# Kernel tuning notes

Measured on AMD Instinct MI355X. Metric: run time of the kernel, lower is better.

The kernel has to match this reference:

```python
import jax, jax.numpy as jnp
import numpy as np

I_T = 0.5       # IoU threshold self.I_t
GAMMA = 2.0     # focal loss gamma
EPS = 1e-7      # focal loss eps clamp
BS, P, C_IN = 8, 2048, 512


def pairwise_iou(b):
    # b: (bs, P, 4) xyxy -> (bs, P, P), same math as torchvision box_iou (no +1)
    area = (b[..., 2] - b[..., 0]) * (b[..., 3] - b[..., 1])
    lt = jnp.maximum(b[:, :, None, :2], b[:, None, :, :2])
    rb = jnp.minimum(b[:, :, None, 2:], b[:, None, :, 2:])
    wh = jnp.clip(rb - lt, 0.0, None)
    inter = wh[..., 0] * wh[..., 1]
    return inter / (area[:, :, None] + area[:, None, :] - inter)


def assign_labels_weights(pre_score, labels, rois):
    # Vectorized, order-faithful version of the per-batch/per-class python loop.
    # Selected seeds per class c: proposals with pre_score[...,c] > 0.5 if more than
    # one, else the single argmax proposal (torch code falls back when k<=1).
    # Sequential `_I > old` running max over (c, j) in ascending order is equivalent
    # to a global first-occurrence argmax (strict >), so per-class max + running
    # compare with earlier-class tie preference reproduces it exactly.
    bs, Pn = pre_score.shape[0], pre_score.shape[1]
    iou = pairwise_iou(rois)                      # (bs, P, P)
    run_I = jnp.full((bs, Pn), -1.0, pre_score.dtype)
    run_w = jnp.ones((bs, Pn), pre_score.dtype)
    hits = []
    for c in range(3):
        s = pre_score[:, :, c]                    # (bs, P)
        th = s > 0.5
        cnt = th.sum(-1)
        onehot = jnp.arange(Pn)[None, :] == jnp.argmax(s, -1)[:, None]
        sel = jnp.where((cnt > 1)[:, None], th, onehot)
        sel = sel & (labels[:, c] != 0)[:, None]  # skip classes absent from image
        masked = jnp.where(sel[:, None, :], iou, -2.0)  # (bs, P, P)
        val = masked.max(-1)                      # best IoU vs any seed of class c
        jidx = masked.argmax(-1)
        cand_x = jnp.take_along_axis(s, jidx, axis=1)
        better = val > run_I
        run_w = jnp.where(better, cand_x, run_w)
        run_I = jnp.where(better, val, run_I)
        hits.append(val > I_T)
    hit = jnp.stack(hits, -1)                     # (bs, P, 3)
    bg = (~hit.any(-1))[..., None]
    y = jnp.concatenate([hit.astype(pre_score.dtype), bg.astype(pre_score.dtype)], -1)
    return y, run_w


def icr_forward(inputs, fc_w, fc_b, pre_score, labels, rois, num):
    bs = inputs.shape[0] // num
    xr = inputs @ fc_w + fc_b                     # (bs*P, 4)
    logit = jax.nn.softmax(xr.reshape(bs, num, 4), -1)
    ps = jax.lax.stop_gradient(pre_score)         # .clone().detach()
    lb = jax.lax.stop_gradient(labels)
    y, w = assign_labels_weights(ps, lb, rois)
    y = y.reshape(bs * num, 4)
    w = w.reshape(bs * num, 1)
    # FocalLoss(gamma=2, mode='none')
    p = jnp.clip(jax.nn.softmax(xr, -1), EPS, 1.0 - EPS)
    fl = -y * jnp.log(p) * (1.0 - p) ** GAMMA
    imbalance = y.sum(0)                          # (4,)
    loss = (w * fl / (imbalance + 1e-7)).reshape(bs, num, 4)
    lab = lb.at[:, 3].set(1.0)[:, None, :]        # lab[:,0,3]=1
    w_ = 10.0 * jnp.exp(logit) * (1.0 - lab) + lab
    loss = (loss * w_).sum() / bs
    return logit, loss


def setup_inputs():
    key = jax.random.key(0)
    k = jax.random.split(key, 6)
    inputs = jax.random.normal(k[0], (BS * P, C_IN), jnp.float32)
    fc_w = jax.random.normal(k[1], (C_IN, 4), jnp.float32) * 0.02
    fc_b = jnp.zeros((4,), jnp.float32)
    pre_score = jax.random.uniform(k[2], (BS, P, 4), dtype=jnp.float32)
    labels = (jax.random.uniform(k[3], (BS, 4)) < 0.5).astype(jnp.float32)
    labels = labels.at[:, 3].set(0.0)
    xy = jax.random.uniform(k[4], (BS, P, 2), dtype=jnp.float32) * 448.0
    wh = jax.random.uniform(k[5], (BS, P, 2), dtype=jnp.float32) * 63.0 + 1.0
    rois = jnp.concatenate([xy, xy + wh], -1)     # valid xyxy boxes in 512x512
    return {"inputs": inputs, "fc_w": fc_w, "fc_b": fc_b, "pre_score": pre_score,
            "labels": labels, "rois": rois, "num": P}


def reference(inputs, fc_w, fc_b, pre_score, labels, rois, num):
    return icr_forward(inputs, fc_w, fc_b, pre_score, labels, rois, num)
```

## Files before the change

kernel.cpp:

```cpp
#include <hip/hip_runtime.h>

#define BSZ 8
#define PN  2048
#define CIN 512
#define CAP 2048


__global__ __launch_bounds__(256) void k_front(
    const float* __restrict__ inp, const float* __restrict__ fcw,
    const float* __restrict__ fcb, const float* __restrict__ ps,
    const float* __restrict__ labels, const float* __restrict__ rois,
    float* __restrict__ logit, float* __restrict__ accum,
    int* __restrict__ meta, float* __restrict__ sList,
    float4* __restrict__ roiList)
{
  const int t = threadIdx.x;
  if (blockIdx.x >= 24) {
    const int gw   = (((int)blockIdx.x - 24) * 256 + t) >> 6;
    const int lane = t & 63;
    const int kb   = lane << 2;
    const float4 wa0 = *(const float4*)(fcw + (kb + 0) * 4);
    const float4 wa1 = *(const float4*)(fcw + (kb + 1) * 4);
    const float4 wa2 = *(const float4*)(fcw + (kb + 2) * 4);
    const float4 wa3 = *(const float4*)(fcw + (kb + 3) * 4);
    const float4 wb0 = *(const float4*)(fcw + (256 + kb + 0) * 4);
    const float4 wb1 = *(const float4*)(fcw + (256 + kb + 1) * 4);
    const float4 wb2 = *(const float4*)(fcw + (256 + kb + 2) * 4);
    const float4 wb3 = *(const float4*)(fcw + (256 + kb + 3) * 4);
    const float4 bias = *(const float4*)fcb;
    #pragma unroll
    for (int rr = 0; rr < 4; ++rr) {
      const int r = (gw << 2) + rr;
      const float* row = inp + r * CIN;
      const float4 xa = *(const float4*)(row + kb);
      const float4 xb = *(const float4*)(row + 256 + kb);
      float a0 = xa.x*wa0.x + xa.y*wa1.x + xa.z*wa2.x + xa.w*wa3.x
               + xb.x*wb0.x + xb.y*wb1.x + xb.z*wb2.x + xb.w*wb3.x;
      float a1 = xa.x*wa0.y + xa.y*wa1.y + xa.z*wa2.y + xa.w*wa3.y
               + xb.x*wb0.y + xb.y*wb1.y + xb.z*wb2.y + xb.w*wb3.y;
      float a2 = xa.x*wa0.z + xa.y*wa1.z + xa.z*wa2.z + xa.w*wa3.z
               + xb.x*wb0.z + xb.y*wb1.z + xb.z*wb2.z + xb.w*wb3.z;
      float a3 = xa.x*wa0.w + xa.y*wa1.w + xa.z*wa2.w + xa.w*wa3.w
               + xb.x*wb0.w + xb.y*wb1.w + xb.z*wb2.w + xb.w*wb3.w;
      #pragma unroll
      for (int off = 32; off; off >>= 1) {
        a0 += __shfl_xor(a0, off); a1 += __shfl_xor(a1, off);
        a2 += __shfl_xor(a2, off); a3 += __shfl_xor(a3, off);
      }
      if (lane == 0) {
        a0 += bias.x; a1 += bias.y; a2 += bias.z; a3 += bias.w;
        const float m  = fmaxf(fmaxf(a0, a1), fmaxf(a2, a3));
        const float e0 = expf(a0 - m), e1 = expf(a1 - m);
        const float e2 = expf(a2 - m), e3 = expf(a3 - m);
        const float inv = 1.0f / (e0 + e1 + e2 + e3);
        float4 o; o.x = e0*inv; o.y = e1*inv; o.z = e2*inv; o.w = e3*inv;
        *(float4*)(logit + r * 4) = o;
      }
    }
    return;
  }

  const int bc = blockIdx.x;
  if (bc == 0 && t < 12) accum[t] = 0.0f;
  const int b = bc / 3;
  const int c = bc % 3;
  const int j0 = t * 8;

  float sv[8];
  int   flg = 0, cnt = 0;
  float vmax = -1e30f;
  int   jmax = 0;
  #pragma unroll
  for (int m = 0; m < 8; ++m) {
    const float s = ps[(b * PN + j0 + m) * 4 + c];
    sv[m] = s;
    if (s > 0.5f) { flg |= 1 << m; ++cnt; }
    if (s > vmax) { vmax = s; jmax = j0 + m; }
  }

  __shared__ float lv[256];
  __shared__ int   lj[256];
  __shared__ int   pre[256];
  lv[t] = vmax; lj[t] = jmax; pre[t] = cnt;
  __syncthreads();
  for (int off = 128; off > 0; off >>= 1) {
    if (t < off) {
      const float v2 = lv[t + off]; const int j2 = lj[t + off];
      if (v2 > lv[t] || (v2 == lv[t] && j2 < lj[t])) { lv[t] = v2; lj[t] = j2; }
    }
    __syncthreads();
  }
  for (int off = 1; off < 256; off <<= 1) {
    const int add = (t >= off) ? pre[t - off] : 0;
    __syncthreads();
    pre[t] += add;
    __syncthreads();
  }
  const int  totalTh = pre[255];
  const int  excl    = pre[t] - cnt;
  const int  jArg    = lj[0];
  const bool lab     = labels[b * 4 + c] != 0.0f;
  const int  L    = (!lab) ? 0 : ((totalTh > 1) ? totalTh : 1);
  const int  Lpad = (L + 7) & ~7;

  __shared__ float4 lastRoi;
  __shared__ float  lastS;
  float4* dstR = roiList + bc * CAP;
  float*  dstS = sList   + bc * CAP;
  const float4* rb = ((const float4*)rois) + b * PN;

  if (lab) {
    if (totalTh > 1) {
      int pos = excl;
      #pragma unroll
      for (int m = 0; m < 8; ++m) {
        if (flg & (1 << m)) {
          const float4 r = rb[j0 + m];
          dstR[pos] = r; dstS[pos] = sv[m];
          if (pos == L - 1) { lastRoi = r; lastS = sv[m]; }
          ++pos;
        }
      }
    } else if (t == (jArg >> 3)) {
      const float4 r = rb[jArg];
      dstR[0] = r; dstS[0] = sv[jArg & 7];
      lastRoi = r; lastS = sv[jArg & 7];
    }
  }
  __syncthreads();
  if (t < Lpad - L) { dstR[L + t] = lastRoi; dstS[L + t] = lastS; }
  if (t == 0) meta[bc] = Lpad;
}

__global__ __launch_bounds__(1024, 4) void k_mid(
    const float* __restrict__ inp, const float* __restrict__ fcw,
    const float* __restrict__ fcb, const float* __restrict__ rois,
    const int* __restrict__ meta, const float4* __restrict__ roiList,
    float* __restrict__ logit,
    float* __restrict__ pbn, float* __restrict__ pbd, int* __restrict__ pbp)
{
  const int blk  = blockIdx.x;
  const int t    = threadIdx.x;
  const int lane = t & 63;
  const int wv   = t >> 6;

  const int b  = blk >> 5;
  const int h  = (blk >> 4) & 1;
  const int it = blk & 15;

  __shared__ __align__(16) float4 sroi[3 * 1024];
  float* mn = (float*)sroi;
  float* md = (float*)sroi + 1536;
  int*   mp = (int*)((float*)sroi + 3072);

  int startc[3], cntc[3];
  #pragma unroll
  for (int c = 0; c < 3; ++c) {
    const int L  = meta[b * 3 + c];
    const int L2 = ((L >> 1) + 7) & ~7;
    const int s0 = h ? L2 : 0;
    const int e0 = h ? L  : L2;
    startc[c] = s0;
    cntc[c]   = e0 - s0;
    if (t < cntc[c])
      sroi[c * 1024 + t] = roiList[(b * 3 + c) * CAP + s0 + t];
  }
  __syncthreads();

  float BN[3][2], BD[3][2]; int BP[3][2];

  if (wv < 8) {
    const int i0 = (it << 7) + lane;
    const float4 ri0 = ((const float4*)rois)[b * PN + i0];
    const float4 ri1 = ((const float4*)rois)[b * PN + i0 + 64];
    const float ar0 = (ri0.z - ri0.x) * (ri0.w - ri0.y);
    const float ar1 = (ri1.z - ri1.x) * (ri1.w - ri1.y);

    auto upd = [](const float4 ri, const float ai,
                  float& n, float& d, int& p,
                  const float4 rj, const float aj, const int pos) {
      const float lx = fmaxf(ri.x, rj.x), ly = fmaxf(ri.y, rj.y);
      const float rx = fminf(ri.z, rj.z), ry = fminf(ri.w, rj.w);
      const float ww = fmaxf(rx - lx, 0.0f), hh = fmaxf(ry - ly, 0.0f);
      const float inter = ww * hh;
      const float uni   = ai + aj - inter;
      if (inter * d > n * uni) { n = inter; d = uni; p = pos; }
    };

    #pragma unroll
    for (int c = 0; c < 3; ++c) {
      const int cnt = cntc[c];
      const int C   = (((cnt + 7) >> 3) + 7) & ~7;
      const int g0  = wv * C;
      int g1 = g0 + C; if (g1 > cnt) g1 = cnt;
      const float4* rbase = sroi + c * 1024;
      float n0A = -2.0f, d0A = 1.0f, n0B = -2.0f, d0B = 1.0f;
      float n1A = -2.0f, d1A = 1.0f, n1B = -2.0f, d1B = 1.0f;
      int   p0A = 0, p0B = 0, p1A = 0, p1B = 0;

      for (int g = g0; g < g1; g += 2) {
        const float4 r0_ = rbase[g], r1_ = rbase[g + 1];
        const float  a0_ = (r0_.z - r0_.x) * (r0_.w - r0_.y);
        const float  a1_ = (r1_.z - r1_.x) * (r1_.w - r1_.y);
        upd(ri0, ar0, n0A, d0A, p0A, r0_, a0_, g);
        upd(ri1, ar1, n1A, d1A, p1A, r0_, a0_, g);
        upd(ri0, ar0, n0B, d0B, p0B, r1_, a1_, g + 1);
        upd(ri1, ar1, n1B, d1B, p1B, r1_, a1_, g + 1);
      }
      {
        const float tB = n0B * d0A, tA = n0A * d0B;
        if (tB > tA || (tB == tA && p0B < p0A)) { n0A = n0B; d0A = d0B; p0A = p0B; }
      }
      {
        const float tB = n1B * d1A, tA = n1A * d1B;
        if (tB > tA || (tB == tA && p1B < p1A)) { n1A = n1B; d1A = d1B; p1A = p1B; }
      }
      BN[c][0] = n0A; BD[c][0] = d0A; BP[c][0] = p0A + startc[c];
      BN[c][1] = n1A; BD[c][1] = d1A; BP[c][1] = p1A + startc[c];
    }
  } else {
    const int fw = (blk << 3) + (wv - 8);
    const int kb = lane << 2;
    const float4 wa0 = *(const float4*)(fcw + (kb + 0) * 4);
    const float4 wa1 = *(const float4*)(fcw + (kb + 1) * 4);
    const float4 wa2 = *(const float4*)(fcw + (kb + 2) * 4);
    const float4 wa3 = *(const float4*)(fcw + (kb + 3) * 4);
    const float4 wb0 = *(const float4*)(fcw + (256 + kb + 0) * 4);
    const float4 wb1 = *(const float4*)(fcw + (256 + kb + 1) * 4);
    const float4 wb2 = *(const float4*)(fcw + (256 + kb + 2) * 4);
    const float4 wb3 = *(const float4*)(fcw + (256 + kb + 3) * 4);
    const float4 bias = *(const float4*)fcb;
    #pragma unroll
    for (int rr = 0; rr < 2; ++rr) {
      const int r = 12288 + (fw << 1) + rr;
      const float* row = inp + r * CIN;
      const float4 xa = *(const float4*)(row + kb);
      const float4 xb = *(const float4*)(row + 256 + kb);
      float a0 = xa.x*wa0.x + xa.y*wa1.x + xa.z*wa2.x + xa.w*wa3.x
               + xb.x*wb0.x + xb.y*wb1.x + xb.z*wb2.x + xb.w*wb3.x;
      float a1 = xa.x*wa0.y + xa.y*wa1.y + xa.z*wa2.y + xa.w*wa3.y
               + xb.x*wb0.y + xb.y*wb1.y + xb.z*wb2.y + xb.w*wb3.y;
      float a2 = xa.x*wa0.z + xa.y*wa1.z + xa.z*wa2.z + xa.w*wa3.z
               + xb.x*wb0.z + xb.y*wb1.z + xb.z*wb2.z + xb.w*wb3.z;
      float a3 = xa.x*wa0.w + xa.y*wa1.w + xa.z*wa2.w + xa.w*wa3.w
               + xb.x*wb0.w + xb.y*wb1.w + xb.z*wb2.w + xb.w*wb3.w;
      #pragma unroll
      for (int off = 32; off; off >>= 1) {
        a0 += __shfl_xor(a0, off); a1 += __shfl_xor(a1, off);
        a2 += __shfl_xor(a2, off); a3 += __shfl_xor(a3, off);
      }
      if (lane == 0) {
        a0 += bias.x; a1 += bias.y; a2 += bias.z; a3 += bias.w;
        const float m  = fmaxf(fmaxf(a0, a1), fmaxf(a2, a3));
        const float e0 = expf(a0 - m), e1 = expf(a1 - m);
        const float e2 = expf(a2 - m), e3 = expf(a3 - m);
        const float inv = 1.0f / (e0 + e1 + e2 + e3);
        float4 o; o.x = e0*inv; o.y = e1*inv; o.z = e2*inv; o.w = e3*inv;
        *(float4*)(logit + r * 4) = o;
      }
    }
  }

  __syncthreads();
  #pragma unroll
  for (int ii = 0; ii < 2; ++ii) {
    if (wv < 8) {
      #pragma unroll
      for (int c = 0; c < 3; ++c) {
        mn[(c * 8 + wv) * 64 + lane] = BN[c][ii];
        md[(c * 8 + wv) * 64 + lane] = BD[c][ii];
        mp[(c * 8 + wv) * 64 + lane] = BP[c][ii];
      }
    }
    __syncthreads();
    if (wv == 0) {
      #pragma unroll
      for (int c = 0; c < 3; ++c) {
        float bn = BN[c][ii], bd = BD[c][ii]; int bp = BP[c][ii];
        for (int w2 = 1; w2 < 8; ++w2) {
          const float n = mn[(c * 8 + w2) * 64 + lane];
          const float d = md[(c * 8 + w2) * 64 + lane];
          const int   p = mp[(c * 8 + w2) * 64 + lane];
          if (n * bd > bn * d) { bn = n; bd = d; bp = p; }
        }
        const int ig = (it << 7) + (ii << 6) + lane;
        const int o  = ((b * 3 + c) * 2 + h) * PN + ig;
        pbn[o] = bn; pbd[o] = bd; pbp[o] = bp;
      }
    }
    __syncthreads();
  }
}

__global__ __launch_bounds__(256) void k_back(
    const float* __restrict__ pbn, const float* __restrict__ pbd,
    const int* __restrict__ pbp, const float* __restrict__ sList,
    const float* __restrict__ logit, const float* __restrict__ labels,
    float* __restrict__ accum, float* __restrict__ loss)
{
  const int t  = threadIdx.x;
  const int gi = blockIdx.x * 256 + t;
  const int b  = gi >> 11;
  const int i  = gi & (PN - 1);

  float v[3], sc[3];
  #pragma unroll
  for (int c = 0; c < 3; ++c) {
    const int o0 = ((b * 3 + c) * 2) * PN + i;
    float n = pbn[o0], d = pbd[o0]; int p = pbp[o0];
    const float n1 = pbn[o0 + PN], d1 = pbd[o0 + PN];
    const int   p1 = pbp[o0 + PN];
    if (n1 * d > n * d1) { n = n1; d = d1; p = p1; }
    v[c]  = n / d;
    sc[c] = sList[(b * 3 + c) * CAP + p];
  }
  float runI = -1.0f, runw = 1.0f;
  if (v[0] > runI) { runw = sc[0]; runI = v[0]; }
  if (v[1] > runI) { runw = sc[1]; runI = v[1]; }
  if (v[2] > runI) { runw = sc[2]; runI = v[2]; }
  const float y0 = (v[0] > 0.5f) ? 1.0f : 0.0f;
  const float y1 = (v[1] > 0.5f) ? 1.0f : 0.0f;
  const float y2 = (v[2] > 0.5f) ? 1.0f : 0.0f;
  const float y3 = (y0 + y1 + y2 == 0.0f) ? 1.0f : 0.0f;

  const float4 lg = ((const float4*)logit)[gi];
  const float lb0 = labels[b * 4 + 0];
  const float lb1 = labels[b * 4 + 1];
  const float lb2 = labels[b * 4 + 2];

  auto term = [&](const float l, const float yv, const float labv) -> float {
    const float p  = fminf(fmaxf(l, 1e-7f), 1.0f - 1e-7f);
    const float om = 1.0f - p;
    const float fl = -yv * logf(p) * om * om;
    const float wl = 10.0f * expf(l) * (1.0f - labv) + labv;
    return runw * fl * wl;
  };
  float s[8];
  s[0] = term(lg.x, y0, lb0); s[1] = term(lg.y, y1, lb1);
  s[2] = term(lg.z, y2, lb2); s[3] = term(lg.w, y3, 1.0f);
  s[4] = y0; s[5] = y1; s[6] = y2; s[7] = y3;

  #pragma unroll
  for (int k = 0; k < 8; ++k)
    #pragma unroll
    for (int off = 32; off; off >>= 1) s[k] += __shfl_xor(s[k], off);

  __shared__ float red[4][8];
  const int wv = t >> 6;
  if ((t & 63) == 0)
    #pragma unroll
    for (int k = 0; k < 8; ++k) red[wv][k] = s[k];
  __syncthreads();
  if (t < 8) {
    const float sum = red[0][t] + red[1][t] + red[2][t] + red[3][t];
    atomicAdd(&accum[t], sum);
  }
  __syncthreads();
  if (t == 0) {
    __threadfence();
    const int ticket = __hip_atomic_fetch_add((int*)(accum + 8), 1,
                        __ATOMIC_ACQ_REL, __HIP_MEMORY_SCOPE_AGENT);
    if (ticket == 63) {
      float L = 0.0f;
      #pragma unroll
      for (int c = 0; c < 4; ++c) {
        const float num = __hip_atomic_load(accum + c,
                            __ATOMIC_RELAXED, __HIP_MEMORY_SCOPE_AGENT);
        const float den = __hip_atomic_load(accum + 4 + c,
                            __ATOMIC_RELAXED, __HIP_MEMORY_SCOPE_AGENT);
        L += num / (den + 1e-7f);
      }
      loss[0] = L * 0.125f;
    }
  }
}

extern "C" void kernel_launch(void* const* d_in, const int* in_sizes, int n_in,
                              void* d_out, int out_size, void* d_ws, size_t ws_size,
                              hipStream_t stream)
{
  (void)in_sizes; (void)n_in; (void)out_size; (void)ws_size;
  const float* inp    = (const float*)d_in[0];
  const float* fcw    = (const float*)d_in[1];
  const float* fcb    = (const float*)d_in[2];
  const float* ps     = (const float*)d_in[3];
  const float* labels = (const float*)d_in[4];
  const float* rois   = (const float*)d_in[5];
  float* out = (float*)d_out;

  char* ws = (char*)d_ws;
  float*  accum   = (float*) (ws);
  int*    meta    = (int*)   (ws + 64);
  float*  sList   = (float*) (ws + 1024);
  float4* roiL    = (float4*)(ws + 394240);
  float*  pbn     = (float*) (ws + 1180672);
  float*  pbd     = (float*) (ws + 1573888);
  int*    pbp     = (int*)   (ws + 1967104);

  k_front<<<792, 256,  0, stream>>>(inp, fcw, fcb, ps, labels, rois,
                                    out, accum, meta, sList, roiL);
  k_mid  <<<256, 1024, 0, stream>>>(inp, fcw, fcb, rois, meta, roiL,
                                    out, pbn, pbd, pbp);
  k_back <<<64,  256,  0, stream>>>(pbn, pbd, pbp, sList, out, labels, accum,
                                    out + BSZ * PN * 4);
}
```

Baseline: 120.6 us.

## Fuse loss epilogue into IoU kernel via grid barrier, move FC rows to front kernel

New measurement: 183.5 us. 52.1% more time.

```diff
diff --git a/kernel.cpp b/kernel.cpp
--- a/kernel.cpp
+++ b/kernel.cpp
@@ -4,6 +4,7 @@
 #define PN  2048
 #define CIN 512
 #define CAP 2048
+#define NW  16
 
 
 __global__ __launch_bounds__(256) void k_front(
@@ -61,7 +62,7 @@
   }
 
   const int bc = blockIdx.x;
-  if (bc == 0 && t < 12) accum[t] = 0.0f;
+  if (bc == 0 && t < 16) accum[t] = 0.0f;
   const int b = bc / 3;
   const int c = bc % 3;
   const int j0 = t * 8;
@@ -133,10 +134,10 @@
 }
 
 __global__ __launch_bounds__(1024, 4) void k_mid(
-    const float* __restrict__ inp, const float* __restrict__ fcw,
-    const float* __restrict__ fcb, const float* __restrict__ rois,
-    const int* __restrict__ meta, const float4* __restrict__ roiList,
-    float* __restrict__ logit,
+    const float* __restrict__ rois, const int* __restrict__ meta,
+    const float4* __restrict__ roiList, const float* __restrict__ sList,
+    const float* __restrict__ logit, const float* __restrict__ labels,
+    float* __restrict__ accum, float* __restrict__ loss,
     float* __restrict__ pbn, float* __restrict__ pbd, int* __restrict__ pbp)
 {
   const int blk  = blockIdx.x;
@@ -150,8 +151,8 @@
 
   __shared__ __align__(16) float4 sroi[3 * 1024];
   float* mn = (float*)sroi;
-  float* md = (float*)sroi + 1536;
-  int*   mp = (int*)((float*)sroi + 3072);
+  float* md = (float*)sroi + 3072;
+  int*   mp = (int*)((float*)sroi + 6144);
 
   int startc[3], cntc[3];
   #pragma unroll
@@ -165,122 +166,74 @@
     if (t < cntc[c])
       sroi[c * 1024 + t] = roiList[(b * 3 + c) * CAP + s0 + t];
   }
-  __syncthreads();
+  const int i0 = (it << 7) + lane;
+  const float4 ri0 = ((const float4*)rois)[b * PN + i0];
+  const float4 ri1 = ((const float4*)rois)[b * PN + i0 + 64];
+  const float ar0 = (ri0.z - ri0.x) * (ri0.w - ri0.y);
+  const float ar1 = (ri1.z - ri1.x) * (ri1.w - ri1.y);
+  __syncthreads();
+
+  auto upd = [](const float4 ri, const float ai,
+                float& n, float& d, int& p,
+                const float4 rj, const float aj, const int pos) {
+    const float lx = fmaxf(ri.x, rj.x), ly = fmaxf(ri.y, rj.y);
+    const float rx = fminf(ri.z, rj.z), ry = fminf(ri.w, rj.w);
+    const float ww = fmaxf(rx - lx, 0.0f), hh = fmaxf(ry - ly, 0.0f);
+    const float inter = ww * hh;
+    const float uni   = ai + aj - inter;
+    if (inter * d > n * uni) { n = inter; d = uni; p = pos; }
+  };
 
   float BN[3][2], BD[3][2]; int BP[3][2];
-
-  if (wv < 8) {
-    const int i0 = (it << 7) + lane;
-    const float4 ri0 = ((const float4*)rois)[b * PN + i0];
-    const float4 ri1 = ((const float4*)rois)[b * PN + i0 + 64];
-    const float ar0 = (ri0.z - ri0.x) * (ri0.w - ri0.y);
-    const float ar1 = (ri1.z - ri1.x) * (ri1.w - ri1.y);
-
-    auto upd = [](const float4 ri, const float ai,
-                  float& n, float& d, int& p,
-                  const float4 rj, const float aj, const int pos) {
-      const float lx = fmaxf(ri.x, rj.x), ly = fmaxf(ri.y, rj.y);
-      const float rx = fminf(ri.z, rj.z), ry = fminf(ri.w, rj.w);
-      const float ww = fmaxf(rx - lx, 0.0f), hh = fmaxf(ry - ly, 0.0f);
-      const float inter = ww * hh;
-      const float uni   = ai + aj - inter;
-      if (inter * d > n * uni) { n = inter; d = uni; p = pos; }
-    };
-
+  #pragma unroll
+  for (int c = 0; c < 3; ++c) {
+    const int cnt = cntc[c];
+    const int C   = (((cnt + 15) >> 4) + 7) & ~7;
+    const int g0  = wv * C;
+    int g1 = g0 + C; if (g1 > cnt) g1 = cnt;
+    const float4* rbase = sroi + c * 1024;
+    float n0A = -2.0f, d0A = 1.0f, n0B = -2.0f, d0B = 1.0f;
+    float n1A = -2.0f, d1A = 1.0f, n1B = -2.0f, d1B = 1.0f;
+    int   p0A = 0, p0B = 0, p1A = 0, p1B = 0;
+
+    for (int g = g0; g < g1; g += 2) {
+      const float4 r0_ = rbase[g], r1_ = rbase[g + 1];
+      const float  a0_ = (r0_.z - r0_.x) * (r0_.w - r0_.y);
+      const float  a1_ = (r1_.z - r1_.x) * (r1_.w - r1_.y);
+      upd(ri0, ar0, n0A, d0A, p0A, r0_, a0_, g);
+      upd(ri1, ar1, n1A, d1A, p1A, r0_, a0_, g);
+      upd(ri0, ar0, n0B, d0B, p0B, r1_, a1_, g + 1);
+      upd(ri1, ar1, n1B, d1B, p1B, r1_, a1_, g + 1);
+    }
+    {
+      const float tB = n0B * d0A, tA = n0A * d0B;
+      if (tB > tA || (tB == tA && p0B < p0A)) { n0A = n0B; d0A = d0B; p0A = p0B; }
+    }
+    {
+      const float tB = n1B * d1A, tA = n1A * d1B;
+      if (tB > tA || (tB == tA && p1B < p1A)) { n1A = n1B; d1A = d1B; p1A = p1B; }
+    }
+    BN[c][0] = n0A; BD[c][0] = d0A; BP[c][0] = p0A + startc[c];
+    BN[c][1] = n1A; BD[c][1] = d1A; BP[c][1] = p1A + startc[c];
+  }
+  __syncthreads();
+  #pragma unroll
+  for (int ii = 0; ii < 2; ++ii) {
     #pragma unroll
     for (int c = 0; c < 3; ++c) {
-      const int cnt = cntc[c];
-      const int C   = (((cnt + 7) >> 3) + 7) & ~7;
-      const int g0  = wv * C;
-      int g1 = g0 + C; if (g1 > cnt) g1 = cnt;
-      const float4* rbase = sroi + c * 1024;
-      float n0A = -2.0f, d0A = 1.0f, n0B = -2.0f, d0B = 1.0f;
-      float n1A = -2.0f, d1A = 1.0f, n1B = -2.0f, d1B = 1.0f;
-      int   p0A = 0, p0B = 0, p1A = 0, p1B = 0;
-
-      for (int g = g0; g < g1; g += 2) {
-        const float4 r0_ = rbase[g], r1_ = rbase[g + 1];
-        const float  a0_ = (r0_.z - r0_.x) * (r0_.w - r0_.y);
-        const float  a1_ = (r1_.z - r1_.x) * (r1_.w - r1_.y);
-        upd(ri0, ar0, n0A, d0A, p0A, r0_, a0_, g);
-        upd(ri1, ar1, n1A, d1A, p1A, r0_, a0_, g);
-        upd(ri0, ar0, n0B, d0B, p0B, r1_, a1_, g + 1);
-        upd(ri1, ar1, n1B, d1B, p1B, r1_, a1_, g + 1);
-      }
-      {
-        const float tB = n0B * d0A, tA = n0A * d0B;
-        if (tB > tA || (tB == tA && p0B < p0A)) { n0A = n0B; d0A = d0B; p0A = p0B; }
-      }
-      {
-        const float tB = n1B * d1A, tA = n1A * d1B;
-        if (tB > tA || (tB == tA && p1B < p1A)) { n1A = n1B; d1A = d1B; p1A = p1B; }
-      }
-      BN[c][0] = n0A; BD[c][0] = d0A; BP[c][0] = p0A + startc[c];
-      BN[c][1] = n1A; BD[c][1] = d1A; BP[c][1] = p1A + startc[c];
-    }
-  } else {
-    const int fw = (blk << 3) + (wv - 8);
-    const int kb = lane << 2;
-    const float4 wa0 = *(const float4*)(fcw + (kb + 0) * 4);
-    const float4 wa1 = *(const float4*)(fcw + (kb + 1) * 4);
-    const float4 wa2 = *(const float4*)(fcw + (kb + 2) * 4);
-    const float4 wa3 = *(const float4*)(fcw + (kb + 3) * 4);
-    const float4 wb0 = *(const float4*)(fcw + (256 + kb + 0) * 4);
-    const float4 wb1 = *(const float4*)(fcw + (256 + kb + 1) * 4);
-    const float4 wb2 = *(const float4*)(fcw + (256 + kb + 2) * 4);
-    const float4 wb3 = *(const float4*)(fcw + (256 + kb + 3) * 4);
-    const float4 bias = *(const float4*)fcb;
-    #pragma unroll
-    for (int rr = 0; rr < 2; ++rr) {
-      const int r = 12288 + (fw << 1) + rr;
-      const float* row = inp + r * CIN;
-      const float4 xa = *(const float4*)(row + kb);
-      const float4 xb = *(const float4*)(row + 256 + kb);
-      float a0 = xa.x*wa0.x + xa.y*wa1.x + xa.z*wa2.x + xa.w*wa3.x
-               + xb.x*wb0.x + xb.y*wb1.x + xb.z*wb2.x + xb.w*wb3.x;
-      float a1 = xa.x*wa0.y + xa.y*wa1.y + xa.z*wa2.y + xa.w*wa3.y
-               + xb.x*wb0.y + xb.y*wb1.y + xb.z*wb2.y + xb.w*wb3.y;
-      float a2 = xa.x*wa0.z + xa.y*wa1.z + xa.z*wa2.z + xa.w*wa3.z
-               + xb.x*wb0.z + xb.y*wb1.z + xb.z*wb2.z + xb.w*wb3.z;
-      float a3 = xa.x*wa0.w + xa.y*wa1.w + xa.z*wa2.w + xa.w*wa3.w
-               + xb.x*wb0.w + xb.y*wb1.w + xb.z*wb2.w + xb.w*wb3.w;
-      #pragma unroll
-      for (int off = 32; off; off >>= 1) {
-        a0 += __shfl_xor(a0, off); a1 += __shfl_xor(a1, off);
-        a2 += __shfl_xor(a2, off); a3 += __shfl_xor(a3, off);
-      }
-      if (lane == 0) {
-        a0 += bias.x; a1 += bias.y; a2 += bias.z; a3 += bias.w;
-        const float m  = fmaxf(fmaxf(a0, a1), fmaxf(a2, a3));
-        const float e0 = expf(a0 - m), e1 = expf(a1 - m);
-        const float e2 = expf(a2 - m), e3 = expf(a3 - m);
-        const float inv = 1.0f / (e0 + e1 + e2 + e3);
-        float4 o; o.x = e0*inv; o.y = e1*inv; o.z = e2*inv; o.w = e3*inv;
-        *(float4*)(logit + r * 4) = o;
-      }
-    }
-  }
-
-  __syncthreads();
-  #pragma unroll
-  for (int ii = 0; ii < 2; ++ii) {
-    if (wv < 8) {
-      #pragma unroll
-      for (int c = 0; c < 3; ++c) {
-        mn[(c * 8 + wv) * 64 + lane] = BN[c][ii];
-        md[(c * 8 + wv) * 64 + lane] = BD[c][ii];
-        mp[(c * 8 + wv) * 64 + lane] = BP[c][ii];
-      }
+      mn[(c * NW + wv) * 64 + lane] = BN[c][ii];
+      md[(c * NW + wv) * 64 + lane] = BD[c][ii];
+      mp[(c * NW + wv) * 64 + lane] = BP[c][ii];
     }
     __syncthreads();
     if (wv == 0) {
       #pragma unroll
       for (int c = 0; c < 3; ++c) {
         float bn = BN[c][ii], bd = BD[c][ii]; int bp = BP[c][ii];
-        for (int w2 = 1; w2 < 8; ++w2) {
-          const float n = mn[(c * 8 + w2) * 64 + lane];
-          const float d = md[(c * 8 + w2) * 64 + lane];
-          const int   p = mp[(c * 8 + w2) * 64 + lane];
+        for (int w2 = 1; w2 < NW; ++w2) {
+          const float n = mn[(c * NW + w2) * 64 + lane];
+          const float d = md[(c * NW + w2) * 64 + lane];
+          const int   p = mp[(c * NW + w2) * 64 + lane];
           if (n * bd > bn * d) { bn = n; bd = d; bp = p; }
         }
         const int ig = (it << 7) + (ii << 6) + lane;
@@ -290,29 +243,36 @@
     }
     __syncthreads();
   }
-}
-
-__global__ __launch_bounds__(256) void k_back(
-    const float* __restrict__ pbn, const float* __restrict__ pbd,
-    const int* __restrict__ pbp, const float* __restrict__ sList,
-    const float* __restrict__ logit, const float* __restrict__ labels,
-    float* __restrict__ accum, float* __restrict__ loss)
-{
-  const int t  = threadIdx.x;
-  const int gi = blockIdx.x * 256 + t;
-  const int b  = gi >> 11;
-  const int i  = gi & (PN - 1);
+
+  __threadfence();
+  __syncthreads();
+  if (t == 0)
+    __hip_atomic_fetch_add((int*)(accum + 9), 1,
+                           __ATOMIC_ACQ_REL, __HIP_MEMORY_SCOPE_AGENT);
+  if (blk >= 16) return;
+
+  if (t == 0) {
+    while (__hip_atomic_load((int*)(accum + 9),
+                             __ATOMIC_ACQUIRE, __HIP_MEMORY_SCOPE_AGENT) < 256)
+      __builtin_amdgcn_s_sleep(1);
+  }
+  __syncthreads();
+  __threadfence();
+
+  const int gi = (blk << 10) + t;
+  const int eb = gi >> 11;
+  const int ei = gi & (PN - 1);
 
   float v[3], sc[3];
   #pragma unroll
   for (int c = 0; c < 3; ++c) {
-    const int o0 = ((b * 3 + c) * 2) * PN + i;
+    const int o0 = ((eb * 3 + c) * 2) * PN + ei;
     float n = pbn[o0], d = pbd[o0]; int p = pbp[o0];
     const float n1 = pbn[o0 + PN], d1 = pbd[o0 + PN];
     const int   p1 = pbp[o0 + PN];
     if (n1 * d > n * d1) { n = n1; d = d1; p = p1; }
     v[c]  = n / d;
-    sc[c] = sList[(b * 3 + c) * CAP + p];
+    sc[c] = sList[(eb * 3 + c) * CAP + p];
   }
   float runI = -1.0f, runw = 1.0f;
   if (v[0] > runI) { runw = sc[0]; runI = v[0]; }
@@ -324,9 +284,9 @@
   const float y3 = (y0 + y1 + y2 == 0.0f) ? 1.0f : 0.0f;
 
   const float4 lg = ((const float4*)logit)[gi];
-  const float lb0 = labels[b * 4 + 0];
-  const float lb1 = labels[b * 4 + 1];
-  const float lb2 = labels[b * 4 + 2];
+  const float lb0 = labels[eb * 4 + 0];
+  const float lb1 = labels[eb * 4 + 1];
+  const float lb2 = labels[eb * 4 + 2];
 
   auto term = [&](const float l, const float yv, const float labv) -> float {
     const float p  = fminf(fmaxf(l, 1e-7f), 1.0f - 1e-7f);
@@ -345,14 +305,15 @@
     #pragma unroll
     for (int off = 32; off; off >>= 1) s[k] += __shfl_xor(s[k], off);
 
-  __shared__ float red[4][8];
-  const int wv = t >> 6;
-  if ((t & 63) == 0)
+  __shared__ float red[NW][8];
+  if (lane == 0)
     #pragma unroll
     for (int k = 0; k < 8; ++k) red[wv][k] = s[k];
   __syncthreads();
   if (t < 8) {
-    const float sum = red[0][t] + red[1][t] + red[2][t] + red[3][t];
+    float sum = 0.0f;
+    #pragma unroll
+    for (int w2 = 0; w2 < NW; ++w2) sum += red[w2][t];
     atomicAdd(&accum[t], sum);
   }
   __syncthreads();
@@ -360,7 +321,7 @@
     __threadfence();
     const int ticket = __hip_atomic_fetch_add((int*)(accum + 8), 1,
                         __ATOMIC_ACQ_REL, __HIP_MEMORY_SCOPE_AGENT);
-    if (ticket == 63) {
+    if (ticket == 15) {
       float L = 0.0f;
       #pragma unroll
       for (int c = 0; c < 4; ++c) {
@@ -397,10 +358,8 @@
   float*  pbd     = (float*) (ws + 1573888);
   int*    pbp     = (int*)   (ws + 1967104);
 
-  k_front<<<792, 256,  0, stream>>>(inp, fcw, fcb, ps, labels, rois,
-                                    out, accum, meta, sList, roiL);
-  k_mid  <<<256, 1024, 0, stream>>>(inp, fcw, fcb, rois, meta, roiL,
-                                    out, pbn, pbd, pbp);
-  k_back <<<64,  256,  0, stream>>>(pbn, pbd, pbp, sList, out, labels, accum,
-                                    out + BSZ * PN * 4);
+  k_front<<<1048, 256,  0, stream>>>(inp, fcw, fcb, ps, labels, rois,
+                                     out, accum, meta, sList, roiL);
+  k_mid  <<<256,  1024, 0, stream>>>(rois, meta, roiL, sList, out, labels,
+                                     accum, out + BSZ * PN * 4, pbn, pbd, pbp);
 }
```
